# Kernel optimization log

Measured on AMD Instinct MI355X. Metric: run time of the kernel, lower is better.

## Reference

```python
import jax, jax.numpy as jnp
import numpy as np
from jax import lax

HIDDEN_DIM = 32
VOCAB_SIZE = 64
B, L = 1024, 2048
LN_EPS = 1e-5
DELTA_EPS = 1e-6


def setup_inputs() -> dict:
    key = jax.random.key(0)
    ks = jax.random.split(key, 12)
    H, V = HIDDEN_DIM, VOCAB_SIZE
    s = 0.02
    return {
        "seq": jax.random.randint(ks[0], (B, L), 0, V),
        "embed": jax.random.normal(ks[1], (V, H), jnp.float32) * s,
        "w1": jax.random.normal(ks[2], (H, 2 * H), jnp.float32) * s,
        "b1": jnp.zeros((2 * H,), jnp.float32),
        "w2": jax.random.normal(ks[3], (2 * H, H), jnp.float32) * s,
        "b2": jnp.zeros((H,), jnp.float32),
        "ln_g": jnp.ones((H,), jnp.float32),
        "ln_b": jnp.zeros((H,), jnp.float32),
        "read_w": jax.random.normal(ks[4], (H, H), jnp.float32) * s,
        "read_b": jnp.zeros((H,), jnp.float32),
        "out_w": jax.random.normal(ks[5], (H, V), jnp.float32) * s,
        "out_b": jnp.zeros((V,), jnp.float32),
    }


def _encode(seq, embed, w1, b1, w2, b2, ln_g, ln_b):
    h = embed[seq]                                   # [B, L, H]
    ff = jnp.maximum(h @ w1 + b1, 0.0) @ w2 + b2     # [B, L, H]
    x = h + ff
    mu = x.mean(-1, keepdims=True)
    var = ((x - mu) ** 2).mean(-1, keepdims=True)
    return (x - mu) * lax.rsqrt(var + LN_EPS) * ln_g + ln_b


def _delta_memory(hidden):
    # hidden: [B, L, H]; sequential delta-rule memory update over first L-1 steps
    Bb, Ll, H = hidden.shape
    keys = jnp.transpose(hidden[:, :-1, :], (1, 0, 2))  # [L-1, B, H]

    def step(M, k):
        # k == v at each step (per original code)
        v_pred = jnp.einsum('bij,bj->bi', M, k)
        denom = (k * k).sum(-1, keepdims=True) + DELTA_EPS
        delta_v = k - v_pred / denom                     # NOTE: v - v_pred/denom, faithful to source
        M = M + delta_v[:, :, None] * k[:, None, :]      # rank-1 outer-product update
        return M, None

    M0 = jnp.zeros((Bb, H, H), hidden.dtype)
    M, _ = lax.scan(step, M0, keys)
    query = hidden[:, -1, :]
    return jnp.einsum('bij,bj->bi', M, query)            # [B, H]


def reference(seq, embed, w1, b1, w2, b2, ln_g, ln_b, read_w, read_b, out_w, out_b):
    hidden = _encode(seq, embed, w1, b1, w2, b2, ln_g, ln_b)
    context = _delta_memory(hidden)
    read = context @ read_w + read_b
    return read @ out_w + out_b                          # [B, VOCAB_SIZE]
```

## Files before the change

kernel.cpp:

```cpp
#include <hip/hip_runtime.h>
#include <math.h>

#define H   32
#define V   64
#define BB  1024
#define LL  2048
#define NKEY 2047

#define OFF_TGE   0
#define OFF_RTOK  32768
#define OFF_ENC   40960
#define OFF_W     50176
#define LDS_TOTAL 58368


__device__ __forceinline__ float frdl(float v, int lane) {
    return __int_as_float(__builtin_amdgcn_readlane(__float_as_int(v), lane));
}

struct TPk { int t0,t1,t2,t3,t4,t5,t6,t7; };
struct GPk { float2 p0,p1,p2,p3,p4,p5,p6,p7; };

__device__ __forceinline__ void tload(TPk& T, const unsigned char* rt, int base8) {
    const uint2 d = *(const uint2*)(rt + base8);
    const unsigned lo = (unsigned)__builtin_amdgcn_readfirstlane((int)d.x);
    const unsigned hi = (unsigned)__builtin_amdgcn_readfirstlane((int)d.y);
    T.t0 = lo & 255; T.t1 = (lo >> 8) & 255; T.t2 = (lo >> 16) & 255; T.t3 = lo >> 24;
    T.t4 = hi & 255; T.t5 = (hi >> 8) & 255; T.t6 = (hi >> 16) & 255; T.t7 = hi >> 24;
}

#define GL1(pk, tk) do { (pk) = *(const float2*)(tgeb + ((tk) << 9) + lane8); } while (0)
__device__ __forceinline__ void gload(GPk& G, const TPk& T,
                                      const char* tgeb, int lane8) {
    GL1(G.p0, T.t0); GL1(G.p1, T.t1); GL1(G.p2, T.t2); GL1(G.p3, T.t3);
    GL1(G.p4, T.t4); GL1(G.p5, T.t5); GL1(G.p6, T.t6); GL1(G.p7, T.t7);
}

#define CH1(pk, tk) do { const float _s = frdl(R, (tk));                    \
                         R = fmaf(_s, (pk).x, R); O = fmaf(_s, (pk).y, O); } while (0)
__device__ __forceinline__ void chain8(const TPk& T, const GPk& G,
                                       float& R, float& O) {
    CH1(G.p0, T.t0); CH1(G.p1, T.t1); CH1(G.p2, T.t2); CH1(G.p3, T.t3);
    CH1(G.p4, T.t4); CH1(G.p5, T.t5); CH1(G.p6, T.t6); CH1(G.p7, T.t7);
}

__global__ __launch_bounds__(256) void fused_kernel(
    const int* __restrict__ seq,
    const float* __restrict__ embed, const float* __restrict__ w1,
    const float* __restrict__ b1,    const float* __restrict__ w2,
    const float* __restrict__ b2,    const float* __restrict__ ln_g,
    const float* __restrict__ ln_b,  const float* __restrict__ read_w,
    const float* __restrict__ read_b,const float* __restrict__ out_w,
    const float* __restrict__ out_b, float* __restrict__ out)
{
    __shared__ __align__(16) char s_mem[LDS_TOTAL];

    const int tid  = threadIdx.x;
    const int lane = tid & 63;
    const int wv   = tid >> 6;
    const int b0   = blockIdx.x * 4;

    int4 pr[8];
#pragma unroll
    for (int u = 0; u < 8; ++u) {
        const int li = u * 256 + tid;
        const int r  = li >> 9;
        const int c4 = li & 511;
        pr[u] = ((const int4*)(seq + (size_t)(b0 + r) * LL))[c4];
    }
    const int wqv = seq[(size_t)(b0 + wv) * LL + (LL - 1)];

    {
        const int av = tid >> 2, sb = tid & 3;
        float h[H], xp[H];
#pragma unroll
        for (int j = 0; j < H; ++j) h[j] = embed[av * H + j];
#pragma unroll
        for (int i = 0; i < H; ++i) xp[i] = (sb == 0) ? (h[i] + b2[i]) : 0.0f;
        for (int m = sb * 16; m < sb * 16 + 16; ++m) {
            float z = b1[m];
#pragma unroll
            for (int j = 0; j < H; ++j) z = fmaf(h[j], w1[j * (2 * H) + m], z);
            z = fmaxf(z, 0.0f);
#pragma unroll
            for (int i = 0; i < H; ++i) xp[i] = fmaf(z, w2[m * H + i], xp[i]);
        }
        float* sp = (float*)(s_mem + OFF_TGE);
#pragma unroll
        for (int i = 0; i < H; ++i) sp[(sb * H + i) * V + av] = xp[i];
    }

    {
        unsigned char* rt8 = (unsigned char*)(s_mem + OFF_RTOK);
#pragma unroll
        for (int u = 0; u < 8; ++u) {
            const int li = u * 256 + tid;
            const int r  = li >> 9;
            const int c0 = (li & 511) * 4;
            const int vals[4] = {pr[u].x, pr[u].y, pr[u].z, pr[u].w};
#pragma unroll
            for (int m = 0; m < 4; ++m) {
                const int c  = c0 + m;
                const int jj = (c == LL - 1) ? (LL - 1) : (LL - 2 - c);
                rt8[r * LL + jj] = (unsigned char)vals[m];
            }
        }
    }

    float ow[H];
#pragma unroll
    for (int j = 0; j < H; ++j) ow[j] = out_w[j * V + lane];
    float O = out_b[lane];
#pragma unroll
    for (int j = 0; j < H; ++j) O = fmaf(read_b[j], ow[j], O);
    {
        float* sW = (float*)(s_mem + OFF_W);
#pragma unroll
        for (int ii = 0; ii < 8; ++ii) {
            const int i = wv * 8 + ii;
            float acc = 0.0f;
#pragma unroll
            for (int j = 0; j < H; ++j) acc = fmaf(read_w[i * H + j], ow[j], acc);
            sW[i * V + lane] = acc;
        }
    }
    __syncthreads();

    if (tid < V) {
        const int v = tid;
        const float* sp = (const float*)(s_mem + OFF_TGE);
        float x[H], mu = 0.0f;
#pragma unroll
        for (int i = 0; i < H; ++i) {
            x[i] = sp[(0 * H + i) * V + v] + sp[(1 * H + i) * V + v] +
                   sp[(2 * H + i) * V + v] + sp[(3 * H + i) * V + v];
            mu += x[i];
        }
        mu *= (1.0f / H);
        float var = 0.0f;
#pragma unroll
        for (int i = 0; i < H; ++i) { float d0 = x[i] - mu; var = fmaf(d0, d0, var); }
        var *= (1.0f / H);
        const float inv = 1.0f / sqrtf(var + 1e-5f);
        float* se = (float*)(s_mem + OFF_ENC);
        float ss = 0.0f;
#pragma unroll
        for (int i = 0; i < H; ++i) {
            float e = (x[i] - mu) * inv * ln_g[i] + ln_b[i];
            se[v * 36 + i] = e;
            ss = fmaf(e, e, ss);
        }
        se[v * 36 + 32] = ss + 1e-6f;
    }
    __syncthreads();

    const float* se = (const float*)(s_mem + OFF_ENC);

    float er[H];
#pragma unroll
    for (int q = 0; q < 8; ++q) {
        const float4 t = *(const float4*)(se + lane * 36 + q * 4);
        er[q * 4 + 0] = t.x; er[q * 4 + 1] = t.y;
        er[q * 4 + 2] = t.z; er[q * 4 + 3] = t.w;
    }
    const float ndv = -1.0f / se[lane * 36 + 32];
    float Wr[H];
    {
        const float* sW = (const float*)(s_mem + OFF_W);
#pragma unroll
        for (int i = 0; i < H; ++i) Wr[i] = sW[i * V + lane];
    }

    {
        float2* tge2 = (float2*)(s_mem + OFF_TGE);
        for (int ww = 0; ww < 16; ++ww) {
            const int w = wv * 16 + ww;
            const float4* ew4 = (const float4*)(se + w * 36);
            float aG = 0.0f, aE = 0.0f;
#pragma unroll
            for (int q = 0; q < 8; ++q) {
                const float4 e4 = ew4[q];
                aG = fmaf(e4.x, er[q * 4 + 0], aG); aE = fmaf(e4.x, Wr[q * 4 + 0], aE);
                aG = fmaf(e4.y, er[q * 4 + 1], aG); aE = fmaf(e4.y, Wr[q * 4 + 1], aE);
                aG = fmaf(e4.z, er[q * 4 + 2], aG); aE = fmaf(e4.z, Wr[q * 4 + 2], aE);
                aG = fmaf(e4.w, er[q * 4 + 3], aG); aE = fmaf(e4.w, Wr[q * 4 + 3], aE);
            }
            float2 pr2; pr2.x = aG * frdl(ndv, w); pr2.y = aE;
            tge2[w * V + lane] = pr2;
        }
    }

    const int wq = __builtin_amdgcn_readfirstlane(wqv);
    float R = 0.0f;
    {
        const float4* q4 = (const float4*)(se + wq * 36);
#pragma unroll
        for (int q = 0; q < 8; ++q) {
            const float4 e4 = q4[q];
            R = fmaf(e4.x, er[q * 4 + 0], R); R = fmaf(e4.y, er[q * 4 + 1], R);
            R = fmaf(e4.z, er[q * 4 + 2], R); R = fmaf(e4.w, er[q * 4 + 3], R);
        }
    }
    __syncthreads();

    const unsigned char* rt   = (const unsigned char*)(s_mem + OFF_RTOK) + wv * LL;
    const char*          tgeb = (const char*)(s_mem + OFF_TGE);
    const int            lane8 = lane << 3;

    TPk T0, T1, T2, T3, TU;
    GPk G0, G1, G2, G3;
    tload(T0, rt, 0); tload(T1, rt, 8); tload(T2, rt, 16);
    gload(G0, T0, tgeb, lane8); gload(G1, T1, tgeb, lane8);

#pragma unroll 1
    for (int P = 0; P < 252; P += 4) {
        gload(G2, T2, tgeb, lane8); tload(T3, rt, (P + 3) * 8); chain8(T0, G0, R, O);
        gload(G3, T3, tgeb, lane8); tload(T0, rt, (P + 4) * 8); chain8(T1, G1, R, O);
        gload(G0, T0, tgeb, lane8); tload(T1, rt, (P + 5) * 8); chain8(T2, G2, R, O);
        gload(G1, T1, tgeb, lane8); tload(T2, rt, (P + 6) * 8); chain8(T3, G3, R, O);
    }
    gload(G2, T2, tgeb, lane8); tload(TU, rt, 2040); chain8(T0, G0, R, O);
    gload(G3, TU, tgeb, lane8);                      chain8(T1, G1, R, O);
    chain8(T2, G2, R, O);
    CH1(G3.p0, TU.t0); CH1(G3.p1, TU.t1); CH1(G3.p2, TU.t2); CH1(G3.p3, TU.t3);
    CH1(G3.p4, TU.t4); CH1(G3.p5, TU.t5); CH1(G3.p6, TU.t6);

    out[(size_t)(b0 + wv) * V + lane] = O;
}

extern "C" void kernel_launch(void* const* d_in, const int* in_sizes, int n_in,
                              void* d_out, int out_size, void* d_ws, size_t ws_size,
                              hipStream_t stream)
{
    const int*   seq    = (const int*)  d_in[0];
    const float* embed  = (const float*)d_in[1];
    const float* w1     = (const float*)d_in[2];
    const float* b1     = (const float*)d_in[3];
    const float* w2     = (const float*)d_in[4];
    const float* b2     = (const float*)d_in[5];
    const float* ln_g   = (const float*)d_in[6];
    const float* ln_b   = (const float*)d_in[7];
    const float* read_w = (const float*)d_in[8];
    const float* read_b = (const float*)d_in[9];
    const float* out_w  = (const float*)d_in[10];
    const float* out_b  = (const float*)d_in[11];

    fused_kernel<<<BB / 4, 256, 0, stream>>>(seq, embed, w1, b1, w2, b2,
                                             ln_g, ln_b, read_w, read_b,
                                             out_w, out_b, (float*)d_out);
}
```

Before: 161.6 us.

## Restructure delta-memory recurrence to shorten readlane dependency chain

```diff
diff --git a/kernel.cpp b/kernel.cpp
--- a/kernel.cpp
+++ b/kernel.cpp
@@ -5,7 +5,6 @@
 #define V   64
 #define BB  1024
 #define LL  2048
-#define NKEY 2047
 
 #define OFF_TGE   0
 #define OFF_RTOK  32768
@@ -14,35 +13,50 @@
 #define LDS_TOTAL 58368
 
 
-__device__ __forceinline__ float frdl(float v, int lane) {
+__device__ __forceinline__ float frdl_f(float v, int lane) {
     return __int_as_float(__builtin_amdgcn_readlane(__float_as_int(v), lane));
 }
-
-struct TPk { int t0,t1,t2,t3,t4,t5,t6,t7; };
-struct GPk { float2 p0,p1,p2,p3,p4,p5,p6,p7; };
-
-__device__ __forceinline__ void tload(TPk& T, const unsigned char* rt, int base8) {
-    const uint2 d = *(const uint2*)(rt + base8);
-    const unsigned lo = (unsigned)__builtin_amdgcn_readfirstlane((int)d.x);
-    const unsigned hi = (unsigned)__builtin_amdgcn_readfirstlane((int)d.y);
-    T.t0 = lo & 255; T.t1 = (lo >> 8) & 255; T.t2 = (lo >> 16) & 255; T.t3 = lo >> 24;
-    T.t4 = hi & 255; T.t5 = (hi >> 8) & 255; T.t6 = (hi >> 16) & 255; T.t7 = hi >> 24;
-}
-
-#define GL1(pk, tk) do { (pk) = *(const float2*)(tgeb + ((tk) << 9) + lane8); } while (0)
-__device__ __forceinline__ void gload(GPk& G, const TPk& T,
-                                      const char* tgeb, int lane8) {
-    GL1(G.p0, T.t0); GL1(G.p1, T.t1); GL1(G.p2, T.t2); GL1(G.p3, T.t3);
-    GL1(G.p4, T.t4); GL1(G.p5, T.t5); GL1(G.p6, T.t6); GL1(G.p7, T.t7);
-}
-
-#define CH1(pk, tk) do { const float _s = frdl(R, (tk));                    \
-                         R = fmaf(_s, (pk).x, R); O = fmaf(_s, (pk).y, O); } while (0)
-__device__ __forceinline__ void chain8(const TPk& T, const GPk& G,
-                                       float& R, float& O) {
-    CH1(G.p0, T.t0); CH1(G.p1, T.t1); CH1(G.p2, T.t2); CH1(G.p3, T.t3);
-    CH1(G.p4, T.t4); CH1(G.p5, T.t5); CH1(G.p6, T.t6); CH1(G.p7, T.t7);
-}
+#define FRDL(x, l) frdl_f((x), (l))
+
+struct TKt { int w0,w1,w2,w3,w4,w5,w6,w7; };
+struct Gt  { float2 p0,p1,p2,p3,p4,p5,p6,p7; };
+
+#define TKEXT(TK, TDv) do {                                                  \
+    const unsigned _lo = (unsigned)__builtin_amdgcn_readfirstlane((int)(TDv).x); \
+    const unsigned _hi = (unsigned)__builtin_amdgcn_readfirstlane((int)(TDv).y); \
+    TK.w0 = _lo & 63; TK.w1 = (_lo >> 8) & 63;                               \
+    TK.w2 = (_lo >> 16) & 63; TK.w3 = (_lo >> 24) & 63;                      \
+    TK.w4 = _hi & 63; TK.w5 = (_hi >> 8) & 63;                               \
+    TK.w6 = (_hi >> 16) & 63; TK.w7 = (_hi >> 24) & 63;                      \
+} while (0)
+
+#define LD2(w_) (*(const float2*)(tgeb + ((w_) << 9) + lane8))
+#define GPF(Gf, TKf) do {                                                    \
+    Gf.p0 = LD2(TKf.w0); Gf.p1 = LD2(TKf.w1); Gf.p2 = LD2(TKf.w2);           \
+    Gf.p3 = LD2(TKf.w3); Gf.p4 = LD2(TKf.w4); Gf.p5 = LD2(TKf.w5);           \
+    Gf.p6 = LD2(TKf.w6); Gf.p7 = LD2(TKf.w7);                                \
+} while (0)
+
+#define PACKF(gpx, Gc, Gf, TKc, TKn, TKf, TDc, DOPF, TDi, offTD, DOTD) do {  \
+    const float c0 = FRDL((gpx),   TKc.w0);                                  \
+    const float c1 = FRDL(Gc.p0.x, TKc.w1);                                  \
+    const float c2 = FRDL(Gc.p1.x, TKc.w2);                                  \
+    const float c3 = FRDL(Gc.p2.x, TKc.w3);                                  \
+    const float c4 = FRDL(Gc.p3.x, TKc.w4);                                  \
+    const float c5 = FRDL(Gc.p4.x, TKc.w5);                                  \
+    const float c6 = FRDL(Gc.p5.x, TKc.w6);                                  \
+    const float c7 = FRDL(Gc.p6.x, TKc.w7);                                  \
+    if (DOPF) { TKEXT(TKf, TDc); GPF(Gf, TKf); }                             \
+    if (DOTD) { TDi = *(const uint2*)(rtw + (offTD)); }                      \
+    s = fmaf(c0, s, avA); O = fmaf(s, Gc.p0.y, O); R = fmaf(s, Gc.p0.x, R); avA = FRDL(R, TKc.w2); \
+    s = fmaf(c1, s, avB); O = fmaf(s, Gc.p1.y, O); R = fmaf(s, Gc.p1.x, R); avB = FRDL(R, TKc.w3); \
+    s = fmaf(c2, s, avA); O = fmaf(s, Gc.p2.y, O); R = fmaf(s, Gc.p2.x, R); avA = FRDL(R, TKc.w4); \
+    s = fmaf(c3, s, avB); O = fmaf(s, Gc.p3.y, O); R = fmaf(s, Gc.p3.x, R); avB = FRDL(R, TKc.w5); \
+    s = fmaf(c4, s, avA); O = fmaf(s, Gc.p4.y, O); R = fmaf(s, Gc.p4.x, R); avA = FRDL(R, TKc.w6); \
+    s = fmaf(c5, s, avB); O = fmaf(s, Gc.p5.y, O); R = fmaf(s, Gc.p5.x, R); avB = FRDL(R, TKc.w7); \
+    s = fmaf(c6, s, avA); O = fmaf(s, Gc.p6.y, O); R = fmaf(s, Gc.p6.x, R); avA = FRDL(R, TKn.w0); \
+    s = fmaf(c7, s, avB); O = fmaf(s, Gc.p7.y, O); R = fmaf(s, Gc.p7.x, R); avB = FRDL(R, TKn.w1); \
+} while (0)
 
 __global__ __launch_bounds__(256) void fused_kernel(
     const int* __restrict__ seq,
@@ -185,7 +199,7 @@
                 aG = fmaf(e4.z, er[q * 4 + 2], aG); aE = fmaf(e4.z, Wr[q * 4 + 2], aE);
                 aG = fmaf(e4.w, er[q * 4 + 3], aG); aE = fmaf(e4.w, Wr[q * 4 + 3], aE);
             }
-            float2 pr2; pr2.x = aG * frdl(ndv, w); pr2.y = aE;
+            float2 pr2; pr2.x = aG * FRDL(ndv, w); pr2.y = aE;
             tge2[w * V + lane] = pr2;
         }
     }
@@ -203,27 +217,60 @@
     }
     __syncthreads();
 
-    const unsigned char* rt   = (const unsigned char*)(s_mem + OFF_RTOK) + wv * LL;
+    const unsigned char* rtw  = (const unsigned char*)(s_mem + OFF_RTOK) + wv * LL;
     const char*          tgeb = (const char*)(s_mem + OFF_TGE);
     const int            lane8 = lane << 3;
 
-    TPk T0, T1, T2, T3, TU;
-    GPk G0, G1, G2, G3;
-    tload(T0, rt, 0); tload(T1, rt, 8); tload(T2, rt, 16);
-    gload(G0, T0, tgeb, lane8); gload(G1, T1, tgeb, lane8);
+    TKt TK0, TK1, TK2, TK3;
+    Gt  G0, G1, G2, G3;
+    uint2 TD0, TD1, TD2, TD3;
+
+    {
+        const uint2 d0 = *(const uint2*)(rtw + 0);
+        const uint2 d1 = *(const uint2*)(rtw + 8);
+        TKEXT(TK0, d0); TKEXT(TK1, d1);
+    }
+    GPF(G0, TK0); GPF(G1, TK1);
+    TD2 = *(const uint2*)(rtw + 16);
+    TD3 = *(const uint2*)(rtw + 24);
+
+    float s  = 0.0f;
+    float gz = 0.0f;
+    float avA = FRDL(R, TK0.w0);
+    float avB = FRDL(R, TK0.w1);
+
+    PACKF(gz,      G0, G2, TK0, TK1, TK2, TD2, 1, TD0, 4 * 8, 1);
+    PACKF(G0.p7.x, G1, G3, TK1, TK2, TK3, TD3, 1, TD1, 5 * 8, 1);
+    PACKF(G1.p7.x, G2, G0, TK2, TK3, TK0, TD0, 1, TD2, 6 * 8, 1);
+    PACKF(G2.p7.x, G3, G1, TK3, TK0, TK1, TD1, 1, TD3, 7 * 8, 1);
 
 #pragma unroll 1
-    for (int P = 0; P < 252; P += 4) {
-        gload(G2, T2, tgeb, lane8); tload(T3, rt, (P + 3) * 8); chain8(T0, G0, R, O);
-        gload(G3, T3, tgeb, lane8); tload(T0, rt, (P + 4) * 8); chain8(T1, G1, R, O);
-        gload(G0, T0, tgeb, lane8); tload(T1, rt, (P + 5) * 8); chain8(T2, G2, R, O);
-        gload(G1, T1, tgeb, lane8); tload(T2, rt, (P + 6) * 8); chain8(T3, G3, R, O);
-    }
-    gload(G2, T2, tgeb, lane8); tload(TU, rt, 2040); chain8(T0, G0, R, O);
-    gload(G3, TU, tgeb, lane8);                      chain8(T1, G1, R, O);
-    chain8(T2, G2, R, O);
-    CH1(G3.p0, TU.t0); CH1(G3.p1, TU.t1); CH1(G3.p2, TU.t2); CH1(G3.p3, TU.t3);
-    CH1(G3.p4, TU.t4); CH1(G3.p5, TU.t5); CH1(G3.p6, TU.t6);
+    for (int P4 = 4; P4 < 252; P4 += 4) {
+        PACKF(G3.p7.x, G0, G2, TK0, TK1, TK2, TD2, 1, TD0, (P4 + 4) * 8, 1);
+        PACKF(G0.p7.x, G1, G3, TK1, TK2, TK3, TD3, 1, TD1, (P4 + 5) * 8, 1);
+        PACKF(G1.p7.x, G2, G0, TK2, TK3, TK0, TD0, 1, TD2, (P4 + 6) * 8, 1);
+        PACKF(G2.p7.x, G3, G1, TK3, TK0, TK1, TD1, 1, TD3, (P4 + 7) * 8, 1);
+    }
+    PACKF(G3.p7.x, G0, G2, TK0, TK1, TK2, TD2, 1, TD0, 0, 0);
+    PACKF(G0.p7.x, G1, G3, TK1, TK2, TK3, TD3, 1, TD1, 0, 0);
+    PACKF(G1.p7.x, G2, G0, TK2, TK3, TK0, TD0, 0, TD2, 0, 0);
+
+    {
+        const float c0 = FRDL(G2.p7.x, TK3.w0);
+        const float c1 = FRDL(G3.p0.x, TK3.w1);
+        const float c2 = FRDL(G3.p1.x, TK3.w2);
+        const float c3 = FRDL(G3.p2.x, TK3.w3);
+        const float c4 = FRDL(G3.p3.x, TK3.w4);
+        const float c5 = FRDL(G3.p4.x, TK3.w5);
+        const float c6 = FRDL(G3.p5.x, TK3.w6);
+        s = fmaf(c0, s, avA); O = fmaf(s, G3.p0.y, O); R = fmaf(s, G3.p0.x, R); avA = FRDL(R, TK3.w2);
+        s = fmaf(c1, s, avB); O = fmaf(s, G3.p1.y, O); R = fmaf(s, G3.p1.x, R); avB = FRDL(R, TK3.w3);
+        s = fmaf(c2, s, avA); O = fmaf(s, G3.p2.y, O); R = fmaf(s, G3.p2.x, R); avA = FRDL(R, TK3.w4);
+        s = fmaf(c3, s, avB); O = fmaf(s, G3.p3.y, O); R = fmaf(s, G3.p3.x, R); avB = FRDL(R, TK3.w5);
+        s = fmaf(c4, s, avA); O = fmaf(s, G3.p4.y, O); R = fmaf(s, G3.p4.x, R); avA = FRDL(R, TK3.w6);
+        s = fmaf(c5, s, avB); O = fmaf(s, G3.p5.y, O); R = fmaf(s, G3.p5.x, R);
+        s = fmaf(c6, s, avA); O = fmaf(s, G3.p6.y, O);
+    }
 
     out[(size_t)(b0 + wv) * V + lane] = O;
 }
```

Result: slower. 178.1 us (+10.2%).

## Process eight batch rows per 512-thread block and overlay token table on encoder LDS

Applied to the files above, without the earlier changes.

```diff
diff --git a/kernel.cpp b/kernel.cpp
--- a/kernel.cpp
+++ b/kernel.cpp
@@ -5,13 +5,14 @@
 #define V   64
 #define BB  1024
 #define LL  2048
-#define NKEY 2047
+
+#define NW  8
+#define NBLK (BB / NW)
 
 #define OFF_TGE   0
 #define OFF_RTOK  32768
-#define OFF_ENC   40960
-#define OFF_W     50176
-#define LDS_TOTAL 58368
+#define OFF_ENC   32768
+#define LDS_TOTAL 49152
 
 
 __device__ __forceinline__ float frdl(float v, int lane) {
@@ -25,18 +26,18 @@
     const uint2 d = *(const uint2*)(rt + base8);
     const unsigned lo = (unsigned)__builtin_amdgcn_readfirstlane((int)d.x);
     const unsigned hi = (unsigned)__builtin_amdgcn_readfirstlane((int)d.y);
-    T.t0 = lo & 255; T.t1 = (lo >> 8) & 255; T.t2 = (lo >> 16) & 255; T.t3 = lo >> 24;
-    T.t4 = hi & 255; T.t5 = (hi >> 8) & 255; T.t6 = (hi >> 16) & 255; T.t7 = hi >> 24;
-}
-
-#define GL1(pk, tk) do { (pk) = *(const float2*)(tgeb + ((tk) << 9) + lane8); } while (0)
+    T.t0 = lo & 63; T.t1 = (lo >> 8) & 63; T.t2 = (lo >> 16) & 63; T.t3 = (lo >> 24) & 63;
+    T.t4 = hi & 63; T.t5 = (hi >> 8) & 63; T.t6 = (hi >> 16) & 63; T.t7 = (hi >> 24) & 63;
+}
+
+#define LD2(w_) (*(const float2*)(tgeb + ((w_) << 9) + lane8))
 __device__ __forceinline__ void gload(GPk& G, const TPk& T,
                                       const char* tgeb, int lane8) {
-    GL1(G.p0, T.t0); GL1(G.p1, T.t1); GL1(G.p2, T.t2); GL1(G.p3, T.t3);
-    GL1(G.p4, T.t4); GL1(G.p5, T.t5); GL1(G.p6, T.t6); GL1(G.p7, T.t7);
-}
-
-#define CH1(pk, tk) do { const float _s = frdl(R, (tk));                    \
+    G.p0 = LD2(T.t0); G.p1 = LD2(T.t1); G.p2 = LD2(T.t2); G.p3 = LD2(T.t3);
+    G.p4 = LD2(T.t4); G.p5 = LD2(T.t5); G.p6 = LD2(T.t6); G.p7 = LD2(T.t7);
+}
+
+#define CH1(pk, tk) do { const float _s = frdl(R, (tk));                     \
                          R = fmaf(_s, (pk).x, R); O = fmaf(_s, (pk).y, O); } while (0)
 __device__ __forceinline__ void chain8(const TPk& T, const GPk& G,
                                        float& R, float& O) {
@@ -44,7 +45,7 @@
     CH1(G.p4, T.t4); CH1(G.p5, T.t5); CH1(G.p6, T.t6); CH1(G.p7, T.t7);
 }
 
-__global__ __launch_bounds__(256) void fused_kernel(
+__global__ __launch_bounds__(512, 2) void fused_kernel(
     const int* __restrict__ seq,
     const float* __restrict__ embed, const float* __restrict__ w1,
     const float* __restrict__ b1,    const float* __restrict__ w2,
@@ -58,19 +59,9 @@
     const int tid  = threadIdx.x;
     const int lane = tid & 63;
     const int wv   = tid >> 6;
-    const int b0   = blockIdx.x * 4;
-
-    int4 pr[8];
-#pragma unroll
-    for (int u = 0; u < 8; ++u) {
-        const int li = u * 256 + tid;
-        const int r  = li >> 9;
-        const int c4 = li & 511;
-        pr[u] = ((const int4*)(seq + (size_t)(b0 + r) * LL))[c4];
-    }
-    const int wqv = seq[(size_t)(b0 + wv) * LL + (LL - 1)];
-
-    {
+    const int b0   = blockIdx.x * NW;
+
+    if (tid < 256) {
         const int av = tid >> 2, sb = tid & 3;
         float h[H], xp[H];
 #pragma unroll
@@ -90,40 +81,21 @@
         for (int i = 0; i < H; ++i) sp[(sb * H + i) * V + av] = xp[i];
     }
 
-    {
-        unsigned char* rt8 = (unsigned char*)(s_mem + OFF_RTOK);
-#pragma unroll
-        for (int u = 0; u < 8; ++u) {
-            const int li = u * 256 + tid;
-            const int r  = li >> 9;
-            const int c0 = (li & 511) * 4;
-            const int vals[4] = {pr[u].x, pr[u].y, pr[u].z, pr[u].w};
-#pragma unroll
-            for (int m = 0; m < 4; ++m) {
-                const int c  = c0 + m;
-                const int jj = (c == LL - 1) ? (LL - 1) : (LL - 2 - c);
-                rt8[r * LL + jj] = (unsigned char)vals[m];
-            }
-        }
-    }
-
     float ow[H];
 #pragma unroll
     for (int j = 0; j < H; ++j) ow[j] = out_w[j * V + lane];
     float O = out_b[lane];
 #pragma unroll
     for (int j = 0; j < H; ++j) O = fmaf(read_b[j], ow[j], O);
-    {
-        float* sW = (float*)(s_mem + OFF_W);
-#pragma unroll
-        for (int ii = 0; ii < 8; ++ii) {
-            const int i = wv * 8 + ii;
-            float acc = 0.0f;
-#pragma unroll
-            for (int j = 0; j < H; ++j) acc = fmaf(read_w[i * H + j], ow[j], acc);
-            sW[i * V + lane] = acc;
-        }
-    }
+    float Wr[H];
+#pragma unroll
+    for (int i = 0; i < H; ++i) {
+        float acc = 0.0f;
+#pragma unroll
+        for (int j = 0; j < H; ++j) acc = fmaf(read_w[i * H + j], ow[j], acc);
+        Wr[i] = acc;
+    }
+    const int wqv = seq[(size_t)(b0 + wv) * LL + (LL - 1)];
     __syncthreads();
 
     if (tid < V) {
@@ -164,17 +136,11 @@
         er[q * 4 + 2] = t.z; er[q * 4 + 3] = t.w;
     }
     const float ndv = -1.0f / se[lane * 36 + 32];
-    float Wr[H];
-    {
-        const float* sW = (const float*)(s_mem + OFF_W);
-#pragma unroll
-        for (int i = 0; i < H; ++i) Wr[i] = sW[i * V + lane];
-    }
 
     {
         float2* tge2 = (float2*)(s_mem + OFF_TGE);
-        for (int ww = 0; ww < 16; ++ww) {
-            const int w = wv * 16 + ww;
+        for (int ww = 0; ww < 8; ++ww) {
+            const int w = wv * 8 + ww;
             const float4* ew4 = (const float4*)(se + w * 36);
             float aG = 0.0f, aE = 0.0f;
 #pragma unroll
@@ -199,6 +165,25 @@
             const float4 e4 = q4[q];
             R = fmaf(e4.x, er[q * 4 + 0], R); R = fmaf(e4.y, er[q * 4 + 1], R);
             R = fmaf(e4.z, er[q * 4 + 2], R); R = fmaf(e4.w, er[q * 4 + 3], R);
+        }
+    }
+    __syncthreads();
+
+    {
+        unsigned char* rt8 = (unsigned char*)(s_mem + OFF_RTOK);
+#pragma unroll
+        for (int u = 0; u < 8; ++u) {
+            const int li = u * 512 + tid;
+            const int r  = li >> 9;
+            const int c0 = (li & 511) * 4;
+            const int4 t4 = ((const int4*)(seq + (size_t)(b0 + r) * LL))[li & 511];
+            const int vals[4] = {t4.x, t4.y, t4.z, t4.w};
+#pragma unroll
+            for (int m = 0; m < 4; ++m) {
+                const int c  = c0 + m;
+                const int jj = (c == LL - 1) ? (LL - 1) : (LL - 2 - c);
+                rt8[r * LL + jj] = (unsigned char)vals[m];
+            }
         }
     }
     __syncthreads();
@@ -245,7 +230,7 @@
     const float* out_w  = (const float*)d_in[10];
     const float* out_b  = (const float*)d_in[11];
 
-    fused_kernel<<<BB / 4, 256, 0, stream>>>(seq, embed, w1, b1, w2, b2,
-                                             ln_g, ln_b, read_w, read_b,
-                                             out_w, out_b, (float*)d_out);
-}
+    fused_kernel<<<NBLK, 512, 0, stream>>>(seq, embed, w1, b1, w2, b2,
+                                           ln_g, ln_b, read_w, read_b,
+                                           out_w, out_b, (float*)d_out);
+}
```

New measurement: 170.3 us. 1.05x slower.
